# Optimization experiments

Measured on AMD Instinct MI355X. Metric: run time of the kernel, lower is better.

Reference implementation:

```python
import jax, jax.numpy as jnp
import numpy as np

B, S, D, H = 8, 1025, 768, 12
HD = D // H  # 64

def setup_inputs() -> dict:
    key = jax.random.key(0)
    ks = jax.random.split(key, 5)
    scale = 0.02
    return {
        "hidden_states": jax.random.normal(ks[0], (B, S, D), jnp.float32),
        "rel_bias": jax.random.normal(ks[1], (1, H, S, S), jnp.float32),
        "Wq": jax.random.normal(ks[2], (D, D), jnp.float32) * scale,
        "bq": jnp.zeros((D,), jnp.float32),
        "Wk": jax.random.normal(ks[3], (D, D), jnp.float32) * scale,
        "bk": jnp.zeros((D,), jnp.float32),
        "Wv": jax.random.normal(ks[4], (D, D), jnp.float32) * scale,
        "bv": jnp.zeros((D,), jnp.float32),
    }

def reference(hidden_states, rel_bias, Wq, bq, Wk, bk, Wv, bv):
    b, s, d = hidden_states.shape
    def split_heads(t):  # [B,S,D] -> [B,H,S,hd]
        return t.reshape(b, s, H, HD).transpose(0, 2, 1, 3)
    q = split_heads(hidden_states @ Wq + bq)
    k = split_heads(hidden_states @ Wk + bk)
    v = split_heads(hidden_states @ Wv + bv)
    inv_sqrt_hd = 1.0 / jnp.sqrt(jnp.asarray(HD, q.dtype))
    scores = jnp.einsum("bhqd,bhkd->bhqk", q, k) * inv_sqrt_hd
    scores = scores + rel_bias  # broadcast [1,H,S,S]
    probs = jax.nn.softmax(scores, axis=-1)
    ctx = jnp.einsum("bhqk,bhkd->bhqd", probs, v)
    out = ctx.transpose(0, 2, 1, 3).reshape(b, s, d)
    return out
```

## Files before the change

### kernel.cpp

```cpp
#include <hip/hip_runtime.h>

using f32x4  = __attribute__((ext_vector_type(4))) float;
using bf16x8 = __attribute__((ext_vector_type(8))) short;

#define SEQ 1025
#define NH  12

__device__ __forceinline__ unsigned short f2bf(float f) {
  unsigned u = __float_as_uint(f);
  u += 0x7FFFu + ((u >> 16) & 1u);
  return (unsigned short)(u >> 16);
}

__device__ __forceinline__ unsigned short f2bf_p(float f) {
  return (unsigned short)((__float_as_uint(f) + 0x8000u) >> 16);
}

__device__ __forceinline__ void async16(const void* g, void* s) {
  __builtin_amdgcn_global_load_lds(
      (const __attribute__((address_space(1))) void*)g,
      (__attribute__((address_space(3))) void*)s, 16, 0, 0);
}

__global__ __launch_bounds__(256) void conv_x(const float* __restrict__ X,
                                              ushort* __restrict__ Xb) {
  int t = blockIdx.x * 256 + threadIdx.x;
  if (t >= 8320 * 96) return;
  int row = t / 96;
  size_t e = (size_t)t * 8;
  union { uint4 q; ushort us[8]; } o;
  if (row < 8200) {
    float4 f0 = *(const float4*)(X + e);
    float4 f1 = *(const float4*)(X + e + 4);
    o.us[0] = f2bf(f0.x); o.us[1] = f2bf(f0.y); o.us[2] = f2bf(f0.z); o.us[3] = f2bf(f0.w);
    o.us[4] = f2bf(f1.x); o.us[5] = f2bf(f1.y); o.us[6] = f2bf(f1.z); o.us[7] = f2bf(f1.w);
  } else {
    o.q = make_uint4(0, 0, 0, 0);
  }
  *(uint4*)(Xb + e) = o.q;
}

__global__ __launch_bounds__(256) void pack_w(const float* __restrict__ Wq,
                                              const float* __restrict__ Wk,
                                              const float* __restrict__ Wv,
                                              ushort* __restrict__ Wt) {
  __shared__ float tile[32][33];
  const int nt = blockIdx.x;
  const int kt = blockIdx.y;
  const int sel = nt / 24;
  const int o0 = (nt - sel * 24) * 32;
  const int k0 = kt * 32;
  const float* W = sel == 0 ? Wq : sel == 1 ? Wk : Wv;
  const int t = threadIdx.x;
  const int x = t & 31, y = t >> 5;
  for (int p = 0; p < 4; ++p)
    tile[y + p * 8][x] = W[(size_t)(k0 + y + p * 8) * 768 + o0 + x];
  __syncthreads();
  for (int p = 0; p < 4; ++p) {
    const int nl = y + p * 8;
    Wt[(size_t)(nt * 32 + nl) * 768 + k0 + x] = f2bf(tile[x][nl]);
  }
}

__global__ __launch_bounds__(256) void pack_bias(const float* __restrict__ bq,
                                                 const float* __restrict__ bk,
                                                 const float* __restrict__ bv,
                                                 float* __restrict__ bc) {
  int t = blockIdx.x * 256 + threadIdx.x;
  if (t < 768) bc[t] = bq[t];
  else if (t < 1536) bc[t] = bk[t - 768];
  else if (t < 2304) bc[t] = bv[t - 1536];
}

__global__ __launch_bounds__(256) void repack_bias(const float* __restrict__ rel,
                                                   float* __restrict__ bt) {
  const int h = blockIdx.x / SEQ;
  const int q = blockIdx.x - h * SEQ;
  const float* src = rel + ((size_t)h * SEQ + q) * SEQ;
  for (int c = threadIdx.x; c < 1088; c += 256) {
    float v = (c <= 1024) ? src[c] * 1.44269504f : -3.0e30f;
    bt[(((size_t)h * 17 + (c >> 6)) * SEQ + q) * 64 + (c & 63)] = v;
  }
}

__global__ __launch_bounds__(256) void gemm_qkv(const ushort* __restrict__ A,
                                                const ushort* __restrict__ Bt,
                                                const float* __restrict__ bias,
                                                ushort* __restrict__ Qo,
                                                ushort* __restrict__ Ko,
                                                ushort* __restrict__ Vo) {
  __shared__ ushort a_sm[128 * 32];
  __shared__ ushort b_sm[128 * 32];
  const int t = threadIdx.x;
  const int lane = t & 63, wave = t >> 6;
  const int quad = lane >> 4, l16 = lane & 15;
  const int wrow = wave >> 1, wcol = wave & 1;
  const int m0 = blockIdx.x * 128, n0 = blockIdx.y * 128;

  f32x4 acc[4][4] = {};

  const ushort* a_g = A + (size_t)m0 * 768;
  const ushort* b_g = Bt + (size_t)n0 * 768;

  for (int k0 = 0; k0 < 768; k0 += 32) {
    __syncthreads();
    for (int r = 0; r < 2; ++r) {
      int c = r * 256 + t;
      int row = c >> 2;
      int colb = (c & 3) * 16;
      async16((const char*)(a_g + (size_t)row * 768 + k0) + colb, (char*)a_sm + c * 16);
      async16((const char*)(b_g + (size_t)row * 768 + k0) + colb, (char*)b_sm + c * 16);
    }
    __syncthreads();
    bf16x8 af[4], bfr[4];
    for (int i = 0; i < 4; ++i) {
      af[i]  = *(const bf16x8*)(a_sm + (wrow * 64 + i * 16 + l16) * 32 + quad * 8);
      bfr[i] = *(const bf16x8*)(b_sm + (wcol * 64 + i * 16 + l16) * 32 + quad * 8);
    }
    for (int i = 0; i < 4; ++i)
      for (int j = 0; j < 4; ++j)
        acc[i][j] = __builtin_amdgcn_mfma_f32_16x16x32_bf16(af[i], bfr[j], acc[i][j], 0, 0, 0);
  }

  for (int j = 0; j < 4; ++j) {
    const int gn = n0 + wcol * 64 + j * 16 + l16;
    const int sel = gn / 768;
    const int o = gn - sel * 768;
    const int hh = o >> 6, hd = o & 63;
    const float bv = bias[gn];
    ushort* dst = sel == 0 ? Qo : sel == 1 ? Ko : Vo;
    for (int i = 0; i < 4; ++i) {
      const int gmb = m0 + wrow * 64 + i * 16 + quad * 4;
      for (int r = 0; r < 4; ++r) {
        const int gm = gmb + r;
        if (gm < 8200) {
          const int bb = gm / 1025;
          const int ss = gm - bb * 1025;
          dst[(((size_t)(bb * NH + hh) * SEQ + ss) << 6) + hd] = f2bf(acc[i][j][r] + bv);
        }
      }
    }
  }
}

__global__ __launch_bounds__(256, 4) void attn(const ushort* __restrict__ Qb,
                                               const ushort* __restrict__ Kb,
                                               const ushort* __restrict__ Vb,
                                               const float* __restrict__ biasT,
                                               float* __restrict__ out) {
  __shared__ char smem[36864];
  ushort* p_sm = (ushort*)smem;
  ushort* k_sm = (ushort*)(smem + 18432);
  ushort* v_sm = (ushort*)(smem + 27648);

  const int t = threadIdx.x;
  const int lane = t & 63, wave = t >> 6;
  const int quad = lane >> 4, l16 = lane & 15;

  const int id = blockIdx.x;
  const int b = id / 108;
  const int g = id - b * 108;
  const int h = g / 9;
  const int qt = g - h * 9;
  const int q0 = qt * 128;

  const size_t bh = (size_t)(b * NH + h) * SEQ * 64;
  const ushort* Qp = Qb + bh;
  const ushort* Kp = Kb + bh;
  const ushort* Vp = Vb + bh;

  uint4 kpre0, kpre1, vpre0, vpre1;
  const int vkp2 = t & 31, vhb = (t >> 5) * 8;

  int rqoff[2][4];
  const int qbase = q0 + wave * 32;
  for (int rt = 0; rt < 2; ++rt)
    for (int r2 = 0; r2 < 4; ++r2) {
      int rq = qbase + rt * 16 + quad * 4 + r2;
      if (rq > 1024) rq = 1024;
      rqoff[rt][r2] = rq * 64;
    }

  auto issue_kv = [&](int kb) {
    {
      int c = t, row = c >> 3, cb = (c & 7) * 8;
      int rk = kb + row; if (rk > 1024) rk = 1024;
      kpre0 = *(const uint4*)(Kp + (size_t)rk * 64 + cb);
    }
    {
      int c = t + 256, row = c >> 3, cb = (c & 7) * 8;
      int rk = kb + row; if (rk > 1024) rk = 1024;
      kpre1 = *(const uint4*)(Kp + (size_t)rk * 64 + cb);
    }
    {
      int r0 = kb + vkp2 * 2;
      int r0c = r0 > 1024 ? 1024 : r0;
      int r1c = r0 + 1 > 1024 ? 1024 : r0 + 1;
      vpre0 = *(const uint4*)(Vp + (size_t)r0c * 64 + vhb);
      vpre1 = *(const uint4*)(Vp + (size_t)r1c * 64 + vhb);
    }
  };

  issue_kv(0);

  ushort* pw = p_sm + wave * (32 * 72);
  for (int i = 0; i < 4; ++i) {
    int c = lane + 64 * i;
    int row = c >> 3, cb = (c & 7) * 8;
    int rq = qbase + row; if (rq > 1024) rq = 1024;
    *(uint4*)(pw + row * 72 + cb) = *(const uint4*)(Qp + (size_t)rq * 64 + cb);
  }
  bf16x8 qf[2][2];
  for (int rt = 0; rt < 2; ++rt)
    for (int ks = 0; ks < 2; ++ks)
      qf[rt][ks] = *(const bf16x8*)(pw + (rt * 16 + l16) * 72 + ks * 32 + quad * 8);

  float lst[8] = {0, 0, 0, 0, 0, 0, 0, 0};
  f32x4 oacc[2][4] = {};
  const float c_scale = 0.18033688f;
  const float* btile0 = biasT + (size_t)h * 17 * (SEQ * 64) + l16;

  for (int kt = 0; kt < 17; ++kt) {
    __syncthreads();
    {
      int c = t;
      *(uint4*)(k_sm + (c >> 3) * 72 + (c & 7) * 8) = kpre0;
      c = t + 256;
      *(uint4*)(k_sm + (c >> 3) * 72 + (c & 7) * 8) = kpre1;
    }
    {
      union { uint4 q; ushort us[8]; } e0, e1;
      e0.q = vpre0; e1.q = vpre1;
      for (int e = 0; e < 8; ++e)
        *(unsigned*)(v_sm + (vhb + e) * 72 + vkp2 * 2) =
            (unsigned)e0.us[e] | ((unsigned)e1.us[e] << 16);
    }
    __syncthreads();

    if (kt < 16) issue_kv(kt * 64 + 64);

    const float* bt = btile0 + (size_t)kt * (SEQ * 64);
    float bpre[2][4][4];
    for (int rt = 0; rt < 2; ++rt)
      for (int ct = 0; ct < 4; ++ct)
        for (int r2 = 0; r2 < 4; ++r2)
          bpre[rt][ct][r2] = bt[rqoff[rt][r2] + ct * 16];

    f32x4 sc[2][4] = {};
    for (int ct = 0; ct < 4; ++ct)
      for (int ks = 0; ks < 2; ++ks) {
        bf16x8 kf = *(const bf16x8*)(k_sm + (ct * 16 + l16) * 72 + ks * 32 + quad * 8);
        sc[0][ct] = __builtin_amdgcn_mfma_f32_16x16x32_bf16(qf[0][ks], kf, sc[0][ct], 0, 0, 0);
        sc[1][ct] = __builtin_amdgcn_mfma_f32_16x16x32_bf16(qf[1][ks], kf, sc[1][ct], 0, 0, 0);
      }

    for (int rt = 0; rt < 2; ++rt)
      for (int ct = 0; ct < 4; ++ct)
        for (int r2 = 0; r2 < 4; ++r2) {
          float p = __builtin_amdgcn_exp2f(
              fmaf(sc[rt][ct][r2], c_scale, bpre[rt][ct][r2]));
          lst[rt * 4 + r2] += p;
          pw[(rt * 16 + quad * 4 + r2) * 72 + ct * 16 + l16] = f2bf_p(p);
        }

    for (int ks = 0; ks < 2; ++ks) {
      bf16x8 pf0 = *(const bf16x8*)(pw + l16 * 72 + ks * 32 + quad * 8);
      bf16x8 pf1 = *(const bf16x8*)(pw + (16 + l16) * 72 + ks * 32 + quad * 8);
      for (int c4 = 0; c4 < 4; ++c4) {
        bf16x8 vf = *(const bf16x8*)(v_sm + (c4 * 16 + l16) * 72 + ks * 32 + quad * 8);
        oacc[0][c4] = __builtin_amdgcn_mfma_f32_16x16x32_bf16(pf0, vf, oacc[0][c4], 0, 0, 0);
        oacc[1][c4] = __builtin_amdgcn_mfma_f32_16x16x32_bf16(pf1, vf, oacc[1][c4], 0, 0, 0);
      }
    }
  }

  for (int si = 0; si < 8; ++si) {
    float s = lst[si];
    s += __shfl_xor(s, 1);
    s += __shfl_xor(s, 2);
    s += __shfl_xor(s, 4);
    s += __shfl_xor(s, 8);
    lst[si] = s;
  }
  for (int rt = 0; rt < 2; ++rt)
    for (int r2 = 0; r2 < 4; ++r2) {
      int s = qbase + rt * 16 + quad * 4 + r2;
      if (s < SEQ) {
        float inv = 1.0f / lst[rt * 4 + r2];
        float* op = out + ((size_t)b * SEQ + s) * 768 + h * 64;
        for (int c4 = 0; c4 < 4; ++c4)
          op[c4 * 16 + l16] = oacc[rt][c4][r2] * inv;
      }
    }
}

extern "C" void kernel_launch(void* const* d_in, const int* in_sizes, int n_in,
                              void* d_out, int out_size, void* d_ws, size_t ws_size,
                              hipStream_t stream) {
  const float* X  = (const float*)d_in[0];
  const float* rb = (const float*)d_in[1];
  const float* Wq = (const float*)d_in[2];
  const float* bq = (const float*)d_in[3];
  const float* Wk = (const float*)d_in[4];
  const float* bk = (const float*)d_in[5];
  const float* Wv = (const float*)d_in[6];
  const float* bv = (const float*)d_in[7];
  float* out = (float*)d_out;
  char* ws = (char*)d_ws;

  ushort* Xb    = (ushort*)ws;
  ushort* Wt    = (ushort*)(ws + 12779520);
  float*  biasc = (float*)(ws + 16318464);
  ushort* Qb    = (ushort*)(ws + 16327680);
  ushort* Kb    = (ushort*)(ws + 16327680 + 12595200);
  ushort* Vb    = (ushort*)(ws + 16327680 + 2 * 12595200);
  float*  biasT = (float*)(ws + 54113280);

  repack_bias<<<NH * SEQ, 256, 0, stream>>>(rb, biasT);
  conv_x<<<3120, 256, 0, stream>>>(X, Xb);
  pack_w<<<dim3(72, 24), 256, 0, stream>>>(Wq, Wk, Wv, Wt);
  pack_bias<<<9, 256, 0, stream>>>(bq, bk, bv, biasc);
  gemm_qkv<<<dim3(65, 18), 256, 0, stream>>>(Xb, Wt, biasc, Qb, Kb, Vb);
  attn<<<864, 256, 0, stream>>>(Qb, Kb, Vb, biasT, out);
}
```

Measured before the change: 365.3 us.

## Repack relative bias into MFMA fragment order and remap attention block order

```diff
diff --git a/kernel.cpp b/kernel.cpp
--- a/kernel.cpp
+++ b/kernel.cpp
@@ -72,14 +72,30 @@
   else if (t < 2304) bc[t] = bv[t - 1536];
 }
 
-__global__ __launch_bounds__(256) void repack_bias(const float* __restrict__ rel,
-                                                   float* __restrict__ bt) {
-  const int h = blockIdx.x / SEQ;
-  const int q = blockIdx.x - h * SEQ;
-  const float* src = rel + ((size_t)h * SEQ + q) * SEQ;
-  for (int c = threadIdx.x; c < 1088; c += 256) {
-    float v = (c <= 1024) ? src[c] * 1.44269504f : -3.0e30f;
-    bt[(((size_t)h * 17 + (c >> 6)) * SEQ + q) * 64 + (c & 63)] = v;
+__global__ __launch_bounds__(256, 2) void repack_bias_frag(
+    const float* __restrict__ rel, float* __restrict__ bf) {
+  __shared__ float lds[16][1092];
+  const int h = blockIdx.x / 72;
+  const int w = blockIdx.x - h * 72;
+  const int t = threadIdx.x;
+  const float* src = rel + (size_t)h * SEQ * SEQ;
+  for (int r = 0; r < 16; ++r) {
+    int q = w * 16 + r; if (q > 1024) q = 1024;
+    const float* row = src + (size_t)q * SEQ;
+    for (int c = t; c < 1088; c += 256)
+      lds[r][c] = (c <= 1024) ? row[c] * 1.44269504f : -3.0e30f;
+  }
+  __syncthreads();
+  float* dst = bf + ((size_t)h * 17 * 72 + w) * 1024;
+  for (int kt = 0; kt < 17; ++kt) {
+    float* d = dst + (size_t)kt * (72 * 1024);
+    for (int j = t; j < 1024; j += 256) {
+      int lane = j >> 4, e = j & 15;
+      int ct = e >> 2, r2 = e & 3;
+      int row = ((lane >> 4) << 2) + r2;
+      int col = kt * 64 + ct * 16 + (lane & 15);
+      d[j] = lds[row][col];
+    }
   }
 }
 
@@ -146,7 +162,7 @@
 __global__ __launch_bounds__(256, 4) void attn(const ushort* __restrict__ Qb,
                                                const ushort* __restrict__ Kb,
                                                const ushort* __restrict__ Vb,
-                                               const float* __restrict__ biasT,
+                                               const float* __restrict__ biasF,
                                                float* __restrict__ out) {
   __shared__ char smem[36864];
   ushort* p_sm = (ushort*)smem;
@@ -158,10 +174,10 @@
   const int quad = lane >> 4, l16 = lane & 15;
 
   const int id = blockIdx.x;
-  const int b = id / 108;
-  const int g = id - b * 108;
-  const int h = g / 9;
-  const int qt = g - h * 9;
+  const int x = id & 7, s = id >> 3;
+  const int Gg = s / 9, qt = s - Gg * 9;
+  const int G = Gg * 8 + x;
+  const int b = G / 12, h = G - b * 12;
   const int q0 = qt * 128;
 
   const size_t bh = (size_t)(b * NH + h) * SEQ * 64;
@@ -171,15 +187,6 @@
 
   uint4 kpre0, kpre1, vpre0, vpre1;
   const int vkp2 = t & 31, vhb = (t >> 5) * 8;
-
-  int rqoff[2][4];
-  const int qbase = q0 + wave * 32;
-  for (int rt = 0; rt < 2; ++rt)
-    for (int r2 = 0; r2 < 4; ++r2) {
-      int rq = qbase + rt * 16 + quad * 4 + r2;
-      if (rq > 1024) rq = 1024;
-      rqoff[rt][r2] = rq * 64;
-    }
 
   auto issue_kv = [&](int kb) {
     {
@@ -204,6 +211,7 @@
   issue_kv(0);
 
   ushort* pw = p_sm + wave * (32 * 72);
+  const int qbase = q0 + wave * 32;
   for (int i = 0; i < 4; ++i) {
     int c = lane + 64 * i;
     int row = c >> 3, cb = (c & 7) * 8;
@@ -218,7 +226,8 @@
   float lst[8] = {0, 0, 0, 0, 0, 0, 0, 0};
   f32x4 oacc[2][4] = {};
   const float c_scale = 0.18033688f;
-  const float* btile0 = biasT + (size_t)h * 17 * (SEQ * 64) + l16;
+  const float* bf_base = biasF +
+      ((size_t)h * 17 * 72 + (qt * 8 + wave * 2)) * 1024 + (lane << 4);
 
   for (int kt = 0; kt < 17; ++kt) {
     __syncthreads();
@@ -237,14 +246,13 @@
     }
     __syncthreads();
 
-    if (kt < 16) issue_kv(kt * 64 + 64);
-
-    const float* bt = btile0 + (size_t)kt * (SEQ * 64);
-    float bpre[2][4][4];
+    const float* bfp = bf_base + (size_t)kt * (72 * 1024);
+    f32x4 br[2][4];
     for (int rt = 0; rt < 2; ++rt)
       for (int ct = 0; ct < 4; ++ct)
-        for (int r2 = 0; r2 < 4; ++r2)
-          bpre[rt][ct][r2] = bt[rqoff[rt][r2] + ct * 16];
+        br[rt][ct] = *(const f32x4*)(bfp + rt * 1024 + ct * 4);
+
+    if (kt < 16) issue_kv(kt * 64 + 64);
 
     f32x4 sc[2][4] = {};
     for (int ct = 0; ct < 4; ++ct)
@@ -258,7 +266,7 @@
       for (int ct = 0; ct < 4; ++ct)
         for (int r2 = 0; r2 < 4; ++r2) {
           float p = __builtin_amdgcn_exp2f(
-              fmaf(sc[rt][ct][r2], c_scale, bpre[rt][ct][r2]));
+              fmaf(sc[rt][ct][r2], c_scale, br[rt][ct][r2]));
           lst[rt * 4 + r2] += p;
           pw[(rt * 16 + quad * 4 + r2) * 72 + ct * 16 + l16] = f2bf_p(p);
         }
@@ -275,19 +283,19 @@
   }
 
   for (int si = 0; si < 8; ++si) {
-    float s = lst[si];
-    s += __shfl_xor(s, 1);
-    s += __shfl_xor(s, 2);
-    s += __shfl_xor(s, 4);
-    s += __shfl_xor(s, 8);
-    lst[si] = s;
+    float s2 = lst[si];
+    s2 += __shfl_xor(s2, 1);
+    s2 += __shfl_xor(s2, 2);
+    s2 += __shfl_xor(s2, 4);
+    s2 += __shfl_xor(s2, 8);
+    lst[si] = s2;
   }
   for (int rt = 0; rt < 2; ++rt)
     for (int r2 = 0; r2 < 4; ++r2) {
-      int s = qbase + rt * 16 + quad * 4 + r2;
-      if (s < SEQ) {
+      int sr = qbase + rt * 16 + quad * 4 + r2;
+      if (sr < SEQ) {
         float inv = 1.0f / lst[rt * 4 + r2];
-        float* op = out + ((size_t)b * SEQ + s) * 768 + h * 64;
+        float* op = out + ((size_t)b * SEQ + sr) * 768 + h * 64;
         for (int c4 = 0; c4 < 4; ++c4)
           op[c4 * 16 + l16] = oacc[rt][c4][r2] * inv;
       }
@@ -308,18 +316,18 @@
   float* out = (float*)d_out;
   char* ws = (char*)d_ws;
 
-  ushort* Xb    = (ushort*)ws;
-  ushort* Wt    = (ushort*)(ws + 12779520);
-  float*  biasc = (float*)(ws + 16318464);
-  ushort* Qb    = (ushort*)(ws + 16327680);
-  ushort* Kb    = (ushort*)(ws + 16327680 + 12595200);
-  ushort* Vb    = (ushort*)(ws + 16327680 + 2 * 12595200);
-  float*  biasT = (float*)(ws + 54113280);
-
-  repack_bias<<<NH * SEQ, 256, 0, stream>>>(rb, biasT);
+  ushort* Qb    = (ushort*)ws;
+  ushort* Kb    = (ushort*)(ws + 12595200);
+  ushort* Vb    = (ushort*)(ws + 25190400);
+  ushort* Xb    = (ushort*)(ws + 37785600);
+  ushort* Wt    = (ushort*)(ws + 50565120);
+  float*  biasc = (float*)(ws + 54104064);
+  float*  biasF = (float*)(ws + 37785600);
+
   conv_x<<<3120, 256, 0, stream>>>(X, Xb);
   pack_w<<<dim3(72, 24), 256, 0, stream>>>(Wq, Wk, Wv, Wt);
   pack_bias<<<9, 256, 0, stream>>>(bq, bk, bv, biasc);
   gemm_qkv<<<dim3(65, 18), 256, 0, stream>>>(Xb, Wt, biasc, Qb, Kb, Vb);
-  attn<<<864, 256, 0, stream>>>(Qb, Kb, Vb, biasT, out);
-}
+  repack_bias_frag<<<NH * 72, 256, 0, stream>>>(rb, biasF);
+  attn<<<864, 256, 0, stream>>>(Qb, Kb, Vb, biasF, out);
+}
```

Measured after the change: 369.6 us. No clear change (+1.2%).
